# Kernel tuning notes

Hardware: AMD Instinct MI355X
Metric: run time of the kernel (lower is better)

Reference implementation:

```python
import jax, jax.numpy as jnp
import numpy as np

TEMPERATURE = 0.07
N_ANCHORS = 256
THRESHOLD = 0.1
EPS_VALID = 1e-6


def setup_inputs() -> dict:
    key = jax.random.key(0)
    kf, kp, ka = jax.random.split(key, 3)
    B, N, D, H, W = 8, 4, 256, 48, 64
    HW = H * W
    # channels-first features, as the module's permute branch expects
    features = jax.random.normal(kf, (B, N, D, H, W), dtype=jnp.float32)
    # uniform[0,1) -> all points valid (norm > 1e-6) and NN dists mostly < threshold
    pointmaps = jax.random.uniform(kp, (B, N, H, W, 3), dtype=jnp.float32)
    # deterministic stand-in for torch.randperm(N_i)[:n_anchors], one per (view pair, batch)
    keys = jax.random.split(ka, (N - 1) * B)
    perm = jax.vmap(lambda k: jax.random.permutation(k, HW)[:N_ANCHORS])(keys)
    anchor_idx = perm.reshape(N - 1, B, N_ANCHORS).astype(jnp.int32)
    return {"features": features, "pointmaps": pointmaps, "anchor_idx": anchor_idx}


def _l2norm(x):
    # F.normalize(dim=-1) semantics
    return x / jnp.clip(jnp.linalg.norm(x, axis=-1, keepdims=True), 1e-12)


def _pair_loss(fi, fj, pi, pj, vi, vj, aidx):
    # fi, fj: [HW, D]; pi, pj: [HW, 3]; vi, vj: [HW] bool; aidx: [A]
    a_pts = pi[aidx]                                   # [A, 3]
    a_feats = fi[aidx]                                 # [A, D]
    # cdist(anchor_pts, pts_j): [A, HW]
    d2 = jnp.sum((a_pts[:, None, :] - pj[None, :, :]) ** 2, axis=-1)
    dists = jnp.sqrt(jnp.maximum(d2, 0.0))
    dists = jnp.where(vj[None, :], dists, jnp.inf)     # invalid j points can't be matched
    pos_idx = jnp.argmin(dists, axis=-1)               # [A]
    min_d = jnp.min(dists, axis=-1)                    # [A]
    valid_a = (min_d < THRESHOLD) & vi[aidx]           # anchor must be valid + matched
    a_n = _l2norm(a_feats)                             # [A, D]
    p_n = _l2norm(fj[pos_idx])                         # [A, D]
    all_n = _l2norm(fj)                                # [HW, D]
    pos_sim = jnp.sum(a_n * p_n, axis=-1) / TEMPERATURE            # [A]
    all_sim = jnp.einsum('ad,jd->aj', a_n, all_n) / TEMPERATURE    # [A, HW]
    all_sim = jnp.where(vj[None, :], all_sim, -jnp.inf)            # mask invalid negatives
    loss_a = -pos_sim + jax.nn.logsumexp(all_sim, axis=-1)         # [A]
    cnt = jnp.sum(valid_a)
    loss_b = jnp.sum(jnp.where(valid_a, loss_a, 0.0)) / jnp.maximum(cnt, 1)
    include = (cnt >= 5) & (jnp.sum(vi) >= 10) & (jnp.sum(vj) >= 10)
    return loss_b, include


def reference(features, pointmaps, anchor_idx):
    if features.shape[-1] != features.shape[-2]:
        features = jnp.transpose(features, (0, 1, 3, 4, 2))  # [B,N,D,H,W] -> [B,N,H,W,D]
    B, N, H, W, D = features.shape
    feats = features.reshape(B, N, H * W, D)
    pts = pointmaps.reshape(B, N, H * W, 3)
    valid = jnp.linalg.norm(pts, axis=-1) > EPS_VALID    # [B, N, HW]
    total = jnp.float32(0.0)
    for v in range(1, N):  # small fixed loop over view pairs (0, v)
        lb, inc = jax.vmap(_pair_loss)(
            feats[:, 0], feats[:, v], pts[:, 0], pts[:, v],
            valid[:, 0], valid[:, v], anchor_idx[v - 1])
        n_inc = jnp.sum(inc)
        pair = jnp.where(n_inc > 0,
                         jnp.sum(jnp.where(inc, lb, 0.0)) / jnp.maximum(n_inc, 1),
                         0.0)
        total = total + pair
    return total / max(N - 1, 1)
```

## Files before the change

### kernel.cpp

```cpp
#include <hip/hip_runtime.h>
#include <math.h>

#define B_ 8
#define N_ 4
#define D_ 256
#define HW_ 3072
#define A_ 256
#define NP_ 3
#define NJT2_ 48
#define NJB_ 96
#define INV_T 14.2857142857142857f
#define LDKH 64

typedef _Float16 half8 __attribute__((ext_vector_type(8)));
typedef _Float16 half2v __attribute__((ext_vector_type(2)));
typedef float f32x4 __attribute__((ext_vector_type(4)));
typedef unsigned uint2v __attribute__((ext_vector_type(2)));

__global__ __launch_bounds__(256) void k_prep_nn(const float* __restrict__ f,
        const float* __restrict__ pts, _Float16* __restrict__ fh,
        unsigned char* __restrict__ valid, int* __restrict__ vcnt_part,
        const int* __restrict__ aidx, int* __restrict__ pos_idx,
        unsigned char* __restrict__ valid_a, int* __restrict__ ticket) {
  __shared__ __align__(16) unsigned tile[4][32 * 32];
  __shared__ float ssql[4][8][4];
  __shared__ float srn[32];
  int tid = threadIdx.x;

  if (blockIdx.x < 96) {
    int j0 = blockIdx.x * 32;
    int bn = blockIdx.y;
    int n = bn & 3;
    int jq = tid & 7;
    int dr = (tid >> 3) & 15;
    int hh = tid >> 7;

    f32x4 rv[2][4];
#pragma unroll
    for (int dtl = 0; dtl < 2; ++dtl) {
      int dt = 2 * hh + dtl;
      const float* fb = f + ((size_t)bn * D_ + dt * 64 + 4 * dr) * HW_ + j0 + 4 * jq;
      rv[dtl][0] = *(const f32x4*)&fb[0];
      rv[dtl][1] = *(const f32x4*)&fb[HW_];
      rv[dtl][2] = *(const f32x4*)&fb[2 * HW_];
      rv[dtl][3] = *(const f32x4*)&fb[3 * HW_];
    }

    float ssq0 = 0.f, ssq1 = 0.f, ssq2 = 0.f, ssq3 = 0.f;
    int p0 = 2 * dr;
#pragma unroll
    for (int dtl = 0; dtl < 2; ++dtl) {
      int dt = 2 * hh + dtl;
      f32x4 r0 = rv[dtl][0], r1 = rv[dtl][1], r2 = rv[dtl][2], r3 = rv[dtl][3];
      ssq0 = fmaf(r0[0], r0[0], fmaf(r1[0], r1[0], fmaf(r2[0], r2[0], fmaf(r3[0], r3[0], ssq0))));
      ssq1 = fmaf(r0[1], r0[1], fmaf(r1[1], r1[1], fmaf(r2[1], r2[1], fmaf(r3[1], r3[1], ssq1))));
      ssq2 = fmaf(r0[2], r0[2], fmaf(r1[2], r1[2], fmaf(r2[2], r2[2], fmaf(r3[2], r3[2], ssq2))));
      ssq3 = fmaf(r0[3], r0[3], fmaf(r1[3], r1[3], fmaf(r2[3], r2[3], fmaf(r3[3], r3[3], ssq3))));
#pragma unroll
      for (int jj = 0; jj < 4; ++jj) {
        int jl = 4 * jq + jj;
        half2v h01, h23;
        h01[0] = (_Float16)r0[jj]; h01[1] = (_Float16)r1[jj];
        h23[0] = (_Float16)r2[jj]; h23[1] = (_Float16)r3[jj];
        unsigned u01 = __builtin_bit_cast(unsigned, h01);
        unsigned u23 = __builtin_bit_cast(unsigned, h23);
        uint2v w;
        if (jj & 1) { w[0] = u23; w[1] = u01; }
        else        { w[0] = u01; w[1] = u23; }
        *(uint2v*)&tile[dt][jl * 32 + (p0 ^ (jl & 30))] = w;
      }
    }
    ssq0 += __shfl_xor(ssq0, 8); ssq0 += __shfl_xor(ssq0, 16); ssq0 += __shfl_xor(ssq0, 32);
    ssq1 += __shfl_xor(ssq1, 8); ssq1 += __shfl_xor(ssq1, 16); ssq1 += __shfl_xor(ssq1, 32);
    ssq2 += __shfl_xor(ssq2, 8); ssq2 += __shfl_xor(ssq2, 16); ssq2 += __shfl_xor(ssq2, 32);
    ssq3 += __shfl_xor(ssq3, 8); ssq3 += __shfl_xor(ssq3, 16); ssq3 += __shfl_xor(ssq3, 32);
    if ((tid & 63) < 8) {
      int w = tid >> 6;
      ssql[w][jq][0] = ssq0; ssql[w][jq][1] = ssq1;
      ssql[w][jq][2] = ssq2; ssql[w][jq][3] = ssq3;
    }
    __syncthreads();
    if (tid < 32) {
      float s = ssql[0][tid >> 2][tid & 3] + ssql[1][tid >> 2][tid & 3]
              + ssql[2][tid >> 2][tid & 3] + ssql[3][tid >> 2][tid & 3];
      float r = 1.f / fmaxf(sqrtf(s), 1e-12f);
      srn[tid] = (n == 0) ? r * INV_T : r;
      size_t idx = (size_t)bn * HW_ + j0 + tid;
      const float* p = pts + idx * 3;
      float x = p[0], y = p[1], z = p[2];
      int v = (x * x + y * y + z * z) > 1e-12f ? 1 : 0;
      valid[idx] = (unsigned char)v;
      unsigned long long mask = __ballot(v);
      if (tid == 0) vcnt_part[bn * NJB_ + blockIdx.x] = __popcll(mask);
    }
    __syncthreads();
    unsigned* outw = (unsigned*)fh;
    int c = tid & 31;
    int jr = tid >> 5;
#pragma unroll
    for (int dt = 0; dt < 4; ++dt) {
#pragma unroll
      for (int pass = 0; pass < 4; ++pass) {
        int j = jr + pass * 8;
        float sc = srn[j];
        unsigned u = tile[dt][j * 32 + (c ^ (j & 31))];
        half2v h = __builtin_bit_cast(half2v, u);
        half2v o;
        o[0] = (_Float16)((float)h[0] * sc);
        o[1] = (_Float16)((float)h[1] * sc);
        outw[((size_t)bn * HW_ + j0 + j) * (D_ / 2) + dt * 32 + c] =
            __builtin_bit_cast(unsigned, o);
      }
    }
  } else {
    int gid = (blockIdx.x - 96) * 32 + blockIdx.y;
    if (gid == 0 && tid == 0) *ticket = 0;
    int wave = tid >> 6, lane = tid & 63;
    int agrp = gid & 63;
    int b = (gid >> 6) & 7;
    int p = gid >> 9;
    int a = agrp * 4 + wave;
    int vv = p + 1;
    int col = aidx[(p * B_ + b) * A_ + a];
    const float* pi = pts + ((size_t)(b * N_) * HW_ + col) * 3;
    float ax = pi[0], ay = pi[1], az = pi[2];
    int vi = (ax * ax + ay * ay + az * az) > 1e-12f ? 1 : 0;
    const f32x4* pj4 = (const f32x4*)(pts + (size_t)(b * N_ + vv) * HW_ * 3);
    float best = INFINITY; int bidx = 0x7fffffff;
#pragma unroll 2
    for (int t = 0; t < HW_ / 256; ++t) {
      int jb = t * 256 + lane * 4;
      int base = t * 192 + lane * 3;
      f32x4 q0 = pj4[base + 0];
      f32x4 q1 = pj4[base + 1];
      f32x4 q2 = pj4[base + 2];
      float px[4] = {q0[0], q0[3], q1[2], q2[1]};
      float py[4] = {q0[1], q1[0], q1[3], q2[2]};
      float pz[4] = {q0[2], q1[1], q2[0], q2[3]};
#pragma unroll
      for (int k = 0; k < 4; ++k) {
        float x = px[k], y = py[k], z = pz[k];
        int vj = (x * x + y * y + z * z) > 1e-12f;
        float dx = ax - x, dy = ay - y, dz = az - z;
        float dist = sqrtf(dx * dx + dy * dy + dz * dz);
        int j = jb + k;
        if (vj && (dist < best || (dist == best && j < bidx))) { best = dist; bidx = j; }
      }
    }
#pragma unroll
    for (int o = 32; o > 0; o >>= 1) {
      float ob = __shfl_xor(best, o);
      int oi = __shfl_xor(bidx, o);
      if (ob < best || (ob == best && oi < bidx)) { best = ob; bidx = oi; }
    }
    if (lane == 0) {
      int ai = (p * B_ + b) * A_ + a;
      pos_idx[ai] = (bidx == 0x7fffffff) ? 0 : bidx;
      valid_a[ai] = (best < 0.1f) && vi;
    }
  }
}

#define STAGE_AB(KK, BUF) do {                                                 \
  _Pragma("unroll")                                                            \
  for (int cc = 0; cc < 4; ++cc) {                                             \
    const _Float16* srcA = fA + (size_t)colA[cc] * D_ + (KK) * 64 + gsw * 8;   \
    __builtin_amdgcn_global_load_lds(                                          \
        (const __attribute__((address_space(1))) void*)srcA,                   \
        (__attribute__((address_space(3))) void*)&As[BUF][(wid * 32 + cc * 8) * LDKH], \
        16, 0, 0);                                                             \
  }                                                                            \
  _Pragma("unroll")                                                            \
  for (int cc = 0; cc < 4; ++cc) {                                             \
    const _Float16* srcB = fB + (size_t)rowB[cc] * D_ + (KK) * 64 + gsw * 8;   \
    __builtin_amdgcn_global_load_lds(                                          \
        (const __attribute__((address_space(1))) void*)srcB,                   \
        (__attribute__((address_space(3))) void*)&Bs[BUF][(wid * 32 + cc * 8) * LDKH], \
        16, 0, 0);                                                             \
  }                                                                            \
} while (0)

__global__ __launch_bounds__(256) void k_gemm(const _Float16* __restrict__ fh,
    const int* __restrict__ aidx, const unsigned char* __restrict__ valid,
    const int* __restrict__ pos_idx, float* __restrict__ possim,
    float2* __restrict__ partials) {
  __shared__ __align__(16) char smem[65536];
  _Float16 (*As)[128 * LDKH] = reinterpret_cast<_Float16 (*)[128 * LDKH]>(smem);
  _Float16 (*Bs)[128 * LDKH] = reinterpret_cast<_Float16 (*)[128 * LDKH]>(smem + 32768);
  float (*scr)[132] = reinterpret_cast<float (*)[132]>(smem);

  int jt = blockIdx.x;
  int pbm = blockIdx.y;
  int pb = pbm >> 1, mt = pbm & 1;
  int b = pb & 7, p = pb >> 3, v = p + 1;
  int tid = threadIdx.x;
  int wid = tid >> 6, lane = tid & 63;
  int wr = wid >> 1, wc = wid & 1;
  int j0 = jt * 128;
  const _Float16* fA = fh + (size_t)(b * N_) * HW_ * D_;
  const _Float16* fB = fh + (size_t)(b * N_ + v) * HW_ * D_;

  int rl = lane >> 3;
  int gl = lane & 7;
  int gsw = gl ^ rl;
  int colA[4];
#pragma unroll
  for (int c = 0; c < 4; ++c)
    colA[c] = aidx[(p * B_ + b) * A_ + mt * 128 + wid * 32 + c * 8 + rl];
  int rowB[4];
#pragma unroll
  for (int c = 0; c < 4; ++c) rowB[c] = j0 + wid * 32 + c * 8 + rl;

  f32x4 acc[4][4];
#pragma unroll
  for (int m = 0; m < 4; ++m)
#pragma unroll
    for (int n = 0; n < 4; ++n) acc[m][n] = (f32x4)0.f;

  int kg = lane >> 4;
  int fr = lane & 15;

  STAGE_AB(0, 0);
  __syncthreads();

#pragma unroll
  for (int kk = 0; kk < 4; ++kk) {
    const int cur = kk & 1;
    if (kk < 3) STAGE_AB(kk + 1, cur ^ 1);
#pragma unroll
    for (int s = 0; s < 2; ++s) {
      half8 af[4], bf[4];
      int G = s * 4 + kg;
#pragma unroll
      for (int m = 0; m < 4; ++m) {
        int row = wr * 64 + m * 16 + fr;
        af[m] = *(half8*)&As[cur][row * LDKH + ((G ^ (row & 7)) << 3)];
      }
#pragma unroll
      for (int n = 0; n < 4; ++n) {
        int row = wc * 64 + n * 16 + fr;
        bf[n] = *(half8*)&Bs[cur][row * LDKH + ((G ^ (row & 7)) << 3)];
      }
      __builtin_amdgcn_s_setprio(1);
#pragma unroll
      for (int m = 0; m < 4; ++m)
#pragma unroll
        for (int n = 0; n < 4; ++n)
          acc[m][n] = __builtin_amdgcn_mfma_f32_16x16x32_f16(af[m], bf[n], acc[m][n], 0, 0, 0);
      __builtin_amdgcn_s_setprio(0);
    }
    if (kk < 3) __syncthreads();
  }

  __syncthreads();

  int vrow = b * N_ + v;
  int a_loc = tid >> 1, h = tid & 1;
  int aig = pb * A_ + mt * 128 + a_loc;
  int pidx = pos_idx[aig];

#pragma unroll
  for (int pss = 0; pss < 2; ++pss) {
    if (wc == pss) {
#pragma unroll
      for (int m = 0; m < 4; ++m)
#pragma unroll
        for (int n = 0; n < 4; ++n)
          *(f32x4*)&scr[n * 16 + fr][wr * 64 + m * 16 + kg * 4] = acc[m][n];
    }
    __syncthreads();
    int jbase = j0 + pss * 64 + h * 32;
    const unsigned* vp = (const unsigned*)(valid + (size_t)vrow * HW_ + jbase);
    unsigned vw[8];
#pragma unroll
    for (int w = 0; w < 8; ++w) vw[w] = vp[w];
    float vv[32];
#pragma unroll
    for (int jj = 0; jj < 32; ++jj) vv[jj] = scr[h * 32 + jj][a_loc];
    float mx = -INFINITY;
#pragma unroll
    for (int jj = 0; jj < 32; ++jj) {
      if ((vw[jj >> 2] >> ((jj & 3) * 8)) & 0xff) mx = fmaxf(mx, vv[jj]);
      if (jbase + jj == pidx) possim[aig] = vv[jj];
    }
    float S = 0.f;
#pragma unroll
    for (int jj = 0; jj < 32; ++jj) {
      if ((vw[jj >> 2] >> ((jj & 3) * 8)) & 0xff) S += __expf(vv[jj] - mx);
    }
    float am = fmaxf(mx, __shfl_xor(mx, 1));
    float Ss = (mx == am) ? S : S * __expf(mx - am);
    Ss += __shfl_xor(Ss, 1);
    if (h == 0) partials[(size_t)aig * NJT2_ + (jt * 2 + pss)] = make_float2(am, Ss);
    __syncthreads();
  }
}

__global__ __launch_bounds__(1024) void k_merge(const float2* __restrict__ partials,
    const float* __restrict__ possim, const unsigned char* __restrict__ valid_a,
    const int* __restrict__ vcnt_part, float* __restrict__ lossb,
    int* __restrict__ incb, int* __restrict__ ticket, float* __restrict__ out) {
  int pb = blockIdx.x;
  int b = pb & 7, p = pb >> 3;
  int tid = threadIdx.x;
  int a = tid >> 2, q = tid & 3;
  int ai = pb * A_ + a;

  __shared__ float ss[16]; __shared__ int sc[16];
  __shared__ int v0c, vvc;
  if (tid == 0) { v0c = 0; vvc = 0; }
  __syncthreads();
  if (tid < NJB_) atomicAdd(&v0c, vcnt_part[(b * N_ + 0) * NJB_ + tid]);
  else if (tid < 2 * NJB_) atomicAdd(&vvc, vcnt_part[(b * N_ + p + 1) * NJB_ + (tid - NJB_)]);

  const float4* pt = (const float4*)partials + (size_t)ai * 24 + q * 6;
  float4 vv4[6];
#pragma unroll
  for (int i = 0; i < 6; ++i) vv4[i] = pt[i];
  float mx = -INFINITY;
#pragma unroll
  for (int i = 0; i < 6; ++i) { mx = fmaxf(mx, vv4[i].x); mx = fmaxf(mx, vv4[i].z); }
  float S = 0.f;
  if (mx != -INFINITY) {
#pragma unroll
    for (int i = 0; i < 6; ++i) {
      S += vv4[i].y * __expf(vv4[i].x - mx);
      S += vv4[i].w * __expf(vv4[i].z - mx);
    }
  }
  float am = mx;
#pragma unroll
  for (int o = 1; o < 4; o <<= 1) am = fmaxf(am, __shfl_xor(am, o));
  float Sg = S * ((mx == am) ? 1.f : __expf(mx - am));
#pragma unroll
  for (int o = 1; o < 4; o <<= 1) Sg += __shfl_xor(Sg, o);

  float contrib = 0.f; int cnt = 0;
  if (q == 0) {
    float lse = (am == -INFINITY) ? -INFINITY : am + logf(Sg);
    if (valid_a[ai]) { contrib = lse - possim[ai]; cnt = 1; }
  }
#pragma unroll
  for (int o = 4; o < 64; o <<= 1) {
    contrib += __shfl_xor(contrib, o);
    cnt += __shfl_xor(cnt, o);
  }
  if ((tid & 63) == 0) { ss[tid >> 6] = contrib; sc[tid >> 6] = cnt; }
  __syncthreads();
  if (tid == 0) {
    float s = 0.f; int c = 0;
#pragma unroll
    for (int i = 0; i < 16; ++i) { s += ss[i]; c += sc[i]; }
    float lb = s / (float)(c > 1 ? c : 1);
    int inc = (c >= 5) && (v0c >= 10) && (vvc >= 10);
    lossb[pb] = lb;
    incb[pb] = inc;
    __threadfence();
    int old = atomicAdd(ticket, 1);
    if (old == NP_ * B_ - 1) {
      __threadfence();
      float total = 0.f;
      for (int pp = 0; pp < NP_; ++pp) {
        float sacc = 0.f; int n = 0;
        for (int bb = 0; bb < B_; ++bb)
          if (incb[pp * B_ + bb]) { sacc += lossb[pp * B_ + bb]; ++n; }
        total += (n > 0) ? sacc / (float)n : 0.f;
      }
      out[0] = total / (float)NP_;
    }
  }
}

extern "C" void kernel_launch(void* const* d_in, const int* in_sizes, int n_in,
                              void* d_out, int out_size, void* d_ws, size_t ws_size,
                              hipStream_t stream) {
  const float* f   = (const float*)d_in[0];
  const float* pts = (const float*)d_in[1];
  const int* aidx  = (const int*)d_in[2];
  float* out = (float*)d_out;

  char* ws = (char*)d_ws;
  _Float16* fh          = (_Float16*)(ws);
  unsigned char* valid  = (unsigned char*)(ws + 50331648);
  int* pos_idx          = (int*)(ws + 50429952);
  unsigned char* valid_a= (unsigned char*)(ws + 50454528);
  float* possim         = (float*)(ws + 50460672);
  float* lossb          = (float*)(ws + 50485248);
  int* incb             = (int*)(ws + 50485376);
  float2* partials      = (float2*)(ws + 50485504);
  int* vcnt_part        = (int*)(ws + 52844800);
  int* ticket           = (int*)(ws + 52857088);

  k_prep_nn<<<dim3(144, 32), 256, 0, stream>>>(f, pts, fh, valid, vcnt_part,
                                               aidx, pos_idx, valid_a, ticket);
  k_gemm<<<dim3(24, NP_ * B_ * 2), 256, 0, stream>>>(fh, aidx, valid, pos_idx, possim, partials);
  k_merge<<<NP_ * B_, 1024, 0, stream>>>(partials, possim, valid_a, vcnt_part, lossb, incb, ticket, out);
}
```

Before: 84.04 us.

## Defer L2 normalization scaling to GEMM epilogue, drop LDS transpose in prep

The prep kernel now writes raw fp16 features directly to global memory without the LDS tile and normalization pass, and stores per-row inverse norms (with 1/T folded in for view 0) to a new global buffer. The GEMM epilogue multiplies each dot product by the anchor and candidate scales before the softmax reduction. This removes a shared-memory round trip and a block barrier from the prep kernel, but the global stores become strided 8-byte writes rather than coalesced rows. fp16 now holds unnormalized values, which changes precision and overflow range. The possim value still comes from scaled vv, so it stays consistent.

```diff
diff --git a/kernel.cpp b/kernel.cpp
--- a/kernel.cpp
+++ b/kernel.cpp
@@ -19,12 +19,11 @@
 
 __global__ __launch_bounds__(256) void k_prep_nn(const float* __restrict__ f,
         const float* __restrict__ pts, _Float16* __restrict__ fh,
+        float* __restrict__ srn_g,
         unsigned char* __restrict__ valid, int* __restrict__ vcnt_part,
         const int* __restrict__ aidx, int* __restrict__ pos_idx,
         unsigned char* __restrict__ valid_a, int* __restrict__ ticket) {
-  __shared__ __align__(16) unsigned tile[4][32 * 32];
   __shared__ float ssql[4][8][4];
-  __shared__ float srn[32];
   int tid = threadIdx.x;
 
   if (blockIdx.x < 96) {
@@ -46,29 +45,30 @@
       rv[dtl][3] = *(const f32x4*)&fb[3 * HW_];
     }
 
-    float ssq0 = 0.f, ssq1 = 0.f, ssq2 = 0.f, ssq3 = 0.f;
-    int p0 = 2 * dr;
 #pragma unroll
     for (int dtl = 0; dtl < 2; ++dtl) {
       int dt = 2 * hh + dtl;
+      f32x4 r0 = rv[dtl][0], r1 = rv[dtl][1], r2 = rv[dtl][2], r3 = rv[dtl][3];
+#pragma unroll
+      for (int jj = 0; jj < 4; ++jj) {
+        half2v a, b2;
+        a[0]  = (_Float16)r0[jj]; a[1]  = (_Float16)r1[jj];
+        b2[0] = (_Float16)r2[jj]; b2[1] = (_Float16)r3[jj];
+        uint2v w;
+        w[0] = __builtin_bit_cast(unsigned, a);
+        w[1] = __builtin_bit_cast(unsigned, b2);
+        *(uint2v*)&fh[((size_t)bn * HW_ + j0 + 4 * jq + jj) * D_ + dt * 64 + 4 * dr] = w;
+      }
+    }
+
+    float ssq0 = 0.f, ssq1 = 0.f, ssq2 = 0.f, ssq3 = 0.f;
+#pragma unroll
+    for (int dtl = 0; dtl < 2; ++dtl) {
       f32x4 r0 = rv[dtl][0], r1 = rv[dtl][1], r2 = rv[dtl][2], r3 = rv[dtl][3];
       ssq0 = fmaf(r0[0], r0[0], fmaf(r1[0], r1[0], fmaf(r2[0], r2[0], fmaf(r3[0], r3[0], ssq0))));
       ssq1 = fmaf(r0[1], r0[1], fmaf(r1[1], r1[1], fmaf(r2[1], r2[1], fmaf(r3[1], r3[1], ssq1))));
       ssq2 = fmaf(r0[2], r0[2], fmaf(r1[2], r1[2], fmaf(r2[2], r2[2], fmaf(r3[2], r3[2], ssq2))));
       ssq3 = fmaf(r0[3], r0[3], fmaf(r1[3], r1[3], fmaf(r2[3], r2[3], fmaf(r3[3], r3[3], ssq3))));
-#pragma unroll
-      for (int jj = 0; jj < 4; ++jj) {
-        int jl = 4 * jq + jj;
-        half2v h01, h23;
-        h01[0] = (_Float16)r0[jj]; h01[1] = (_Float16)r1[jj];
-        h23[0] = (_Float16)r2[jj]; h23[1] = (_Float16)r3[jj];
-        unsigned u01 = __builtin_bit_cast(unsigned, h01);
-        unsigned u23 = __builtin_bit_cast(unsigned, h23);
-        uint2v w;
-        if (jj & 1) { w[0] = u23; w[1] = u01; }
-        else        { w[0] = u01; w[1] = u23; }
-        *(uint2v*)&tile[dt][jl * 32 + (p0 ^ (jl & 30))] = w;
-      }
     }
     ssq0 += __shfl_xor(ssq0, 8); ssq0 += __shfl_xor(ssq0, 16); ssq0 += __shfl_xor(ssq0, 32);
     ssq1 += __shfl_xor(ssq1, 8); ssq1 += __shfl_xor(ssq1, 16); ssq1 += __shfl_xor(ssq1, 32);
@@ -84,33 +84,14 @@
       float s = ssql[0][tid >> 2][tid & 3] + ssql[1][tid >> 2][tid & 3]
               + ssql[2][tid >> 2][tid & 3] + ssql[3][tid >> 2][tid & 3];
       float r = 1.f / fmaxf(sqrtf(s), 1e-12f);
-      srn[tid] = (n == 0) ? r * INV_T : r;
       size_t idx = (size_t)bn * HW_ + j0 + tid;
+      srn_g[idx] = (n == 0) ? r * INV_T : r;
       const float* p = pts + idx * 3;
       float x = p[0], y = p[1], z = p[2];
       int v = (x * x + y * y + z * z) > 1e-12f ? 1 : 0;
       valid[idx] = (unsigned char)v;
       unsigned long long mask = __ballot(v);
       if (tid == 0) vcnt_part[bn * NJB_ + blockIdx.x] = __popcll(mask);
-    }
-    __syncthreads();
-    unsigned* outw = (unsigned*)fh;
-    int c = tid & 31;
-    int jr = tid >> 5;
-#pragma unroll
-    for (int dt = 0; dt < 4; ++dt) {
-#pragma unroll
-      for (int pass = 0; pass < 4; ++pass) {
-        int j = jr + pass * 8;
-        float sc = srn[j];
-        unsigned u = tile[dt][j * 32 + (c ^ (j & 31))];
-        half2v h = __builtin_bit_cast(half2v, u);
-        half2v o;
-        o[0] = (_Float16)((float)h[0] * sc);
-        o[1] = (_Float16)((float)h[1] * sc);
-        outw[((size_t)bn * HW_ + j0 + j) * (D_ / 2) + dt * 32 + c] =
-            __builtin_bit_cast(unsigned, o);
-      }
     }
   } else {
     int gid = (blockIdx.x - 96) * 32 + blockIdx.y;
@@ -181,9 +162,9 @@
 } while (0)
 
 __global__ __launch_bounds__(256) void k_gemm(const _Float16* __restrict__ fh,
-    const int* __restrict__ aidx, const unsigned char* __restrict__ valid,
-    const int* __restrict__ pos_idx, float* __restrict__ possim,
-    float2* __restrict__ partials) {
+    const float* __restrict__ srn_g, const int* __restrict__ aidx,
+    const unsigned char* __restrict__ valid, const int* __restrict__ pos_idx,
+    float* __restrict__ possim, float2* __restrict__ partials) {
   __shared__ __align__(16) char smem[65536];
   _Float16 (*As)[128 * LDKH] = reinterpret_cast<_Float16 (*)[128 * LDKH]>(smem);
   _Float16 (*Bs)[128 * LDKH] = reinterpret_cast<_Float16 (*)[128 * LDKH]>(smem + 32768);
@@ -258,6 +239,8 @@
   int a_loc = tid >> 1, h = tid & 1;
   int aig = pb * A_ + mt * 128 + a_loc;
   int pidx = pos_idx[aig];
+  int colAe = aidx[(p * B_ + b) * A_ + mt * 128 + a_loc];
+  float sA = srn_g[(size_t)(b * N_) * HW_ + colAe];
 
 #pragma unroll
   for (int pss = 0; pss < 2; ++pss) {
@@ -274,9 +257,14 @@
     unsigned vw[8];
 #pragma unroll
     for (int w = 0; w < 8; ++w) vw[w] = vp[w];
+    float sB[32];
+#pragma unroll
+    for (int q4 = 0; q4 < 8; ++q4)
+      *(f32x4*)&sB[q4 * 4] = *(const f32x4*)&srn_g[(size_t)vrow * HW_ + jbase + q4 * 4];
     float vv[32];
 #pragma unroll
-    for (int jj = 0; jj < 32; ++jj) vv[jj] = scr[h * 32 + jj][a_loc];
+    for (int jj = 0; jj < 32; ++jj)
+      vv[jj] = scr[h * 32 + jj][a_loc] * sA * sB[jj];
     float mx = -INFINITY;
 #pragma unroll
     for (int jj = 0; jj < 32; ++jj) {
@@ -390,9 +378,11 @@
   float2* partials      = (float2*)(ws + 50485504);
   int* vcnt_part        = (int*)(ws + 52844800);
   int* ticket           = (int*)(ws + 52857088);
-
-  k_prep_nn<<<dim3(144, 32), 256, 0, stream>>>(f, pts, fh, valid, vcnt_part,
+  float* srn_g          = (float*)(ws + 52857216);
+
+  k_prep_nn<<<dim3(144, 32), 256, 0, stream>>>(f, pts, fh, srn_g, valid, vcnt_part,
                                                aidx, pos_idx, valid_a, ticket);
-  k_gemm<<<dim3(24, NP_ * B_ * 2), 256, 0, stream>>>(fh, aidx, valid, pos_idx, possim, partials);
+  k_gemm<<<dim3(24, NP_ * B_ * 2), 256, 0, stream>>>(fh, srn_g, aidx, valid, pos_idx,
+                                                     possim, partials);
   k_merge<<<NP_ * B_, 1024, 0, stream>>>(partials, possim, valid_a, vcnt_part, lossb, incb, ticket, out);
 }
```

Result: slower. 89.03 us (+5.9%).
